# Optimization experiments

Measured on AMD Instinct MI355X. Metric: run time of the kernel, lower is better.

## Reference

```python
import jax, jax.numpy as jnp
import numpy as np

B, T, C, H = 2, 2048, 1024, 16
HD = C // H  # head dim = 64


def setup_inputs() -> dict:
    key = jax.random.key(0)
    k0, k1, k2 = jax.random.split(key, 3)
    x = jax.random.normal(k0, (B, T, C), jnp.float32)
    W_attn = jax.random.normal(k1, (C, 3 * C), jnp.float32) * 0.02
    b_attn = jnp.zeros((3 * C,), jnp.float32)
    W_proj = jax.random.normal(k2, (C, C), jnp.float32) * 0.02
    b_proj = jnp.zeros((C,), jnp.float32)
    # rope: (1,1,T,HD//2,2,2) stack of 2x2 rotation matrices [[cos,-sin],[sin,cos]]
    inv_freq = 1.0 / (10000.0 ** (jnp.arange(0, HD, 2, dtype=jnp.float32) / HD))
    ang = jnp.arange(T, dtype=jnp.float32)[:, None] * inv_freq[None, :]  # (T, HD//2)
    cos, sin = jnp.cos(ang), jnp.sin(ang)
    rope = jnp.stack([jnp.stack([cos, -sin], -1), jnp.stack([sin, cos], -1)], -2)
    rope = rope[None, None]  # (1,1,T,HD//2,2,2)
    return dict(x=x, W_attn=W_attn, b_attn=b_attn, W_proj=W_proj, b_proj=b_proj, rope=rope)


def reference(x, W_attn, b_attn, W_proj, b_proj, rope):
    Bv, Tv, Cv = x.shape
    Hd = Cv // H
    qkv = x @ W_attn + b_attn                      # (B,T,3C) fused QKV proj
    q, k, v = jnp.split(qkv, 3, axis=-1)

    def heads(t):
        return t.reshape(Bv, Tv, H, Hd).transpose(0, 2, 1, 3)  # (B,H,T,Hd)

    q, k, v = heads(q), heads(k), heads(v)

    cos = rope[..., 0, 0][..., None]               # (1,1,T,Hd//2,1)
    sin = rope[..., 1, 0][..., None]

    def rot(t):
        tr = t.reshape(Bv, H, Tv, Hd // 2, 2)
        xr, yr = tr[..., 0:1], tr[..., 1:2]
        out = jnp.concatenate([xr * cos - yr * sin, xr * sin + yr * cos], axis=-1)
        return out.reshape(Bv, H, Tv, Hd)

    q, k = rot(q), rot(k)

    scale = 1.0 / np.sqrt(Hd).astype(np.float32)
    att = jnp.einsum('bhqd,bhkd->bhqk', q, k) * scale
    mask = jnp.tril(jnp.ones((Tv, Tv), dtype=bool))  # causal
    att = jnp.where(mask[None, None], att, -jnp.inf)
    att = jax.nn.softmax(att, axis=-1)
    y = jnp.einsum('bhqk,bhkd->bhqd', att, v)
    y = y.transpose(0, 2, 1, 3).reshape(Bv, Tv, Cv)
    return y @ W_proj + b_proj
```

## Files before the change

### kernel.cpp

```cpp
#include <hip/hip_runtime.h>
#include <hip/hip_bf16.h>

typedef __attribute__((ext_vector_type(8))) short short8;
typedef __attribute__((ext_vector_type(4))) short short4b;
typedef __attribute__((ext_vector_type(4))) float f32x4;
typedef __attribute__((ext_vector_type(16))) float f32x16;
typedef __attribute__((ext_vector_type(4))) unsigned u32x4;

static constexpr int Bb = 2, Tt = 2048, Cc = 1024, Hh = 16;
static constexpr int BT = Bb * Tt;
static constexpr int N1 = 3 * Cc;
static constexpr float QS = 0.125f * 1.44269504f;

__device__ __forceinline__ unsigned short f2b(float f) {
  union { float f; unsigned u; } v; v.f = f;
  unsigned r = v.u + 0x7fffu + ((v.u >> 16) & 1u);
  return (unsigned short)(r >> 16);
}
__device__ __forceinline__ float b2f(short s) {
  union { unsigned u; float f; } v; v.u = ((unsigned)(unsigned short)s) << 16;
  return v.f;
}

__global__ __launch_bounds__(256) void k_cast(const float* __restrict__ in,
                                              unsigned short* __restrict__ out, int n) {
  int i = (blockIdx.x * 256 + threadIdx.x) * 8;
  if (i >= n) return;
  float4 a = *reinterpret_cast<const float4*>(in + i);
  float4 b = *reinterpret_cast<const float4*>(in + i + 4);
  short8 o;
  o[0] = f2b(a.x); o[1] = f2b(a.y); o[2] = f2b(a.z); o[3] = f2b(a.w);
  o[4] = f2b(b.x); o[5] = f2b(b.y); o[6] = f2b(b.z); o[7] = f2b(b.w);
  *reinterpret_cast<short8*>(out + i) = o;
}

__global__ __launch_bounds__(256) void k_tcast(const float* __restrict__ in,
                                               unsigned short* __restrict__ out,
                                               int R, int Ccol) {
  __shared__ float tile[32][33];
  int cb = blockIdx.x * 32, rb = blockIdx.y * 32;
  int tx = threadIdx.x & 31, ty = threadIdx.x >> 5;
  for (int i = 0; i < 32; i += 8)
    tile[ty + i][tx] = in[(size_t)(rb + ty + i) * Ccol + cb + tx];
  __syncthreads();
  for (int i = 0; i < 32; i += 8)
    out[(size_t)(cb + ty + i) * R + rb + tx] = f2b(tile[tx][ty + i]);
}

template <int NF, int EPI>
__global__ __launch_bounds__(512, 2)
void k_gemm8(const unsigned short* __restrict__ A, const unsigned short* __restrict__ Bt,
             const float* __restrict__ bias, void* __restrict__ Cout,
             const float* __restrict__ rope, unsigned short* __restrict__ Qs,
             unsigned short* __restrict__ Ks, unsigned short* __restrict__ Vt,
             int M, int N, int K) {
  constexpr int BN = NF * 64;
  constexpr int ASZ = 256 * 64;
  constexpr int BSZ = BN * 64;
  constexpr int STRIDE = ASZ + BSZ;
  extern __shared__ unsigned short lds[];
  const int tid = threadIdx.x, lane = tid & 63, w = tid >> 6;
  const int wm = w >> 2, wn = w & 3;
  const int l15 = lane & 15, l4 = lane >> 4;
  int nbx = gridDim.x;
  int lin = blockIdx.y * nbx + blockIdx.x;
  int cpx = (nbx * gridDim.y) >> 3;
  lin = (lin & 7) * cpx + (lin >> 3);
  const int mb = lin / nbx, nb = lin % nbx;
  const size_t arow0 = (size_t)mb * 256;
  const size_t brow0 = (size_t)nb * BN;

  const int srow = lane >> 3;
  const int scol = (((lane & 7) * 16) ^ (srow << 4)) >> 1;
  auto stage = [&](int buf, int k0) {
    unsigned short* Ab = lds + buf * STRIDE;
    unsigned short* Bb = Ab + ASZ;
#pragma unroll
    for (int i = 0; i < 4; i++) {
      int c = w + 8 * i;
      const unsigned short* g = A + (arow0 + c * 8 + srow) * (size_t)K + k0 + scol;
      __builtin_amdgcn_global_load_lds((const __attribute__((address_space(1))) void*)g,
          (__attribute__((address_space(3))) void*)(Ab + c * 512), 16, 0, 0);
    }
#pragma unroll
    for (int i = 0; i < NF; i++) {
      int c = w + 8 * i;
      const unsigned short* g = Bt + (brow0 + c * 8 + srow) * (size_t)K + k0 + scol;
      __builtin_amdgcn_global_load_lds((const __attribute__((address_space(1))) void*)g,
          (__attribute__((address_space(3))) void*)(Bb + c * 512), 16, 0, 0);
    }
  };

  f32x4 acc[8][NF] = {};
  const int NK = K >> 6;

  stage(0, 0);
  asm volatile("s_waitcnt vmcnt(0)" ::: "memory");
  asm volatile("s_barrier" ::: "memory");

  for (int kt = 0; kt < NK; kt++) {
    int buf = kt & 1;
    if (kt + 1 < NK) stage(buf ^ 1, (kt + 1) << 6);
    const unsigned short* Ab = lds + buf * STRIDE;
    const unsigned short* Bb = Ab + ASZ;
    short8 af[8][2];
#pragma unroll
    for (int p = 0; p < NF; p++) {
      if (p == 0) {
#pragma unroll
        for (int m = 0; m < 8; m++) {
          int ra = wm * 128 + m * 16 + l15;
#pragma unroll
          for (int kk = 0; kk < 2; kk++) {
            int cb = (kk * 64 + l4 * 16) ^ ((ra & 7) << 4);
            af[m][kk] = *reinterpret_cast<const short8*>(Ab + ra * 64 + (cb >> 1));
          }
        }
      }
      short8 bfr[2];
      int rb = wn * (NF * 16) + p * 16 + l15;
#pragma unroll
      for (int kk = 0; kk < 2; kk++) {
        int cb = (kk * 64 + l4 * 16) ^ ((rb & 7) << 4);
        bfr[kk] = *reinterpret_cast<const short8*>(Bb + rb * 64 + (cb >> 1));
      }
      asm volatile("s_barrier" ::: "memory");
      asm volatile("s_waitcnt lgkmcnt(0)" ::: "memory");
      __builtin_amdgcn_sched_barrier(0);
      __builtin_amdgcn_s_setprio(1);
#pragma unroll
      for (int m = 0; m < 8; m++) {
        acc[m][p] = __builtin_amdgcn_mfma_f32_16x16x32_bf16(af[m][0], bfr[0], acc[m][p], 0, 0, 0);
        acc[m][p] = __builtin_amdgcn_mfma_f32_16x16x32_bf16(af[m][1], bfr[1], acc[m][p], 0, 0, 0);
      }
      __builtin_amdgcn_s_setprio(0);
      if (p == NF - 1)
        asm volatile("s_waitcnt vmcnt(0)" ::: "memory");
      asm volatile("s_barrier" ::: "memory");
    }
  }

#pragma unroll
  for (int m = 0; m < 8; m++) {
#pragma unroll
    for (int n = 0; n < NF; n++) {
      int ccol0 = nb * BN + wn * (NF * 16) + n * 16;
      float bv = bias[ccol0 + l15];
      int r0 = mb * 256 + wm * 128 + m * 16 + l4 * 4;
      if (EPI == 0) {
#pragma unroll
        for (int j = 0; j < 4; j++)
          ((float*)Cout)[(size_t)(r0 + j) * N + ccol0 + l15] = acc[m][n][j] + bv;
      } else {
        int cls = ccol0 >> 10;
        int h = (ccol0 >> 6) & 15;
        int d = (ccol0 & 63) + l15;
        int bq = r0 >> 11;
        int t0 = r0 & 2047;
        size_t bh = (size_t)bq * 16 + h;
        if (cls == 2) {
          short4b o;
#pragma unroll
          for (int j = 0; j < 4; j++) o[j] = (short)f2b(acc[m][n][j] + bv);
          *reinterpret_cast<short4b*>(Vt + (bh * 64 + d) * Tt + t0) = o;
        } else {
          unsigned short* dst = (cls == 0) ? Qs : Ks;
          int jj = d >> 1;
          int odd = d & 1;
#pragma unroll
          for (int j = 0; j < 4; j++) {
            float v = acc[m][n][j] + bv;
            float part = __shfl_xor(v, 1);
            float2 sc = *reinterpret_cast<const float2*>(
                rope + (size_t)(t0 + j) * 128 + jj * 4 + 2);
            float x = odd ? part : v;
            float y = odd ? v : part;
            float rot = odd ? (x * sc.x + y * sc.y)
                            : (x * sc.y - y * sc.x);
            if (cls == 0) rot *= QS;
            dst[(bh * Tt + (t0 + j)) * 64 + d] = f2b(rot);
          }
        }
      }
    }
  }
}

__device__ __forceinline__ float tmax16(const f32x16& v) {
  float a0 = fmaxf(v[0], v[1]),   a1 = fmaxf(v[2], v[3]);
  float a2 = fmaxf(v[4], v[5]),   a3 = fmaxf(v[6], v[7]);
  float a4 = fmaxf(v[8], v[9]),   a5 = fmaxf(v[10], v[11]);
  float a6 = fmaxf(v[12], v[13]), a7 = fmaxf(v[14], v[15]);
  float b0 = fmaxf(a0, a1), b1 = fmaxf(a2, a3), b2 = fmaxf(a4, a5), b3 = fmaxf(a6, a7);
  return fmaxf(fmaxf(b0, b1), fmaxf(b2, b3));
}

template <bool DIAG>
__device__ __forceinline__ void attn_tile128(
    const unsigned short* Kl, const unsigned short* Vl,
    int w, int l31, int hi, const short8 qf[4],
    float& m_run, float& l_run, f32x16 oacc[2]) {
  const int ktmax = DIAG ? w : 3;
  f32x16 s[4];
#pragma unroll
  for (int kt = 0; kt < 4; kt++) {
    if (kt > ktmax) continue;
    f32x16 acc = {};
    int rk = kt * 32 + l31;
    int sw = (rk & 7) << 4;
    const unsigned short* krow = Kl + rk * 64;
    short8 kf[4];
#pragma unroll
    for (int kk = 0; kk < 4; kk++)
      kf[kk] = *reinterpret_cast<const short8*>(krow + (((kk * 32 + hi * 16) ^ sw) >> 1));
    __builtin_amdgcn_s_setprio(1);
#pragma unroll
    for (int kk = 0; kk < 4; kk++)
      acc = __builtin_amdgcn_mfma_f32_32x32x16_bf16(kf[kk], qf[kk], acc, 0, 0, 0);
    __builtin_amdgcn_s_setprio(0);
    if (DIAG && kt == w) {
#pragma unroll
      for (int r = 0; r < 16; r++) {
        int e = (r & 3) + 8 * (r >> 2) + 4 * hi;
        if (e > l31) acc[r] = -1e30f;
      }
    }
    s[kt] = acc;
  }
  float km[4];
#pragma unroll
  for (int kt = 0; kt < 4; kt++) km[kt] = (kt <= ktmax) ? tmax16(s[kt]) : -1e30f;
  float mx = fmaxf(fmaxf(km[0], km[1]), fmaxf(km[2], km[3]));
  mx = fmaxf(mx, __shfl_xor(mx, 32));

  float fsc = 1.f;
  if (!__all(mx <= m_run + 8.f)) {
    float nm = fmaxf(m_run, mx);
    fsc = __builtin_amdgcn_exp2f(m_run - nm);
    m_run = nm;
#pragma unroll
    for (int dt = 0; dt < 2; dt++)
#pragma unroll
      for (int r = 0; r < 16; r++) oacc[dt][r] *= fsc;
  }

  float kps[4] = {0.f, 0.f, 0.f, 0.f};
#pragma unroll
  for (int kt = 0; kt < 4; kt++) {
    if (kt > ktmax) continue;
    float p[16];
#pragma unroll
    for (int r = 0; r < 16; r++) p[r] = __builtin_amdgcn_exp2f(s[kt][r] - m_run);
    float s0 = (p[0] + p[1]) + (p[2] + p[3]);
    float s1 = (p[4] + p[5]) + (p[6] + p[7]);
    float s2 = (p[8] + p[9]) + (p[10] + p[11]);
    float s3 = (p[12] + p[13]) + (p[14] + p[15]);
    kps[kt] = (s0 + s1) + (s2 + s3);
    unsigned P[8];
#pragma unroll
    for (int i = 0; i < 8; i++)
      asm("v_cvt_pk_bf16_f32 %0, %1, %2" : "=v"(P[i]) : "v"(p[2 * i]), "v"(p[2 * i + 1]));
    unsigned Y0 = (unsigned)__shfl_xor((int)(hi ? P[0] : P[2]), 32);
    unsigned Y1 = (unsigned)__shfl_xor((int)(hi ? P[1] : P[3]), 32);
    unsigned Y2 = (unsigned)__shfl_xor((int)(hi ? P[4] : P[6]), 32);
    unsigned Y3 = (unsigned)__shfl_xor((int)(hi ? P[5] : P[7]), 32);
    u32x4 c0 = hi ? u32x4{Y0, Y1, P[2], P[3]} : u32x4{P[0], P[1], Y0, Y1};
    u32x4 c1 = hi ? u32x4{Y2, Y3, P[6], P[7]} : u32x4{P[4], P[5], Y2, Y3};
    short8 pf0 = __builtin_bit_cast(short8, c0);
    short8 pf1 = __builtin_bit_cast(short8, c1);
#pragma unroll
    for (int dt = 0; dt < 2; dt++) {
      int d = dt * 32 + l31;
      int sv = (d & 15) << 4;
      const unsigned short* vrow = Vl + d * 128;
      short8 vf0 = *reinterpret_cast<const short8*>(vrow + (((kt * 64 + hi * 16) ^ sv) >> 1));
      short8 vf1 = *reinterpret_cast<const short8*>(vrow + (((kt * 64 + 32 + hi * 16) ^ sv) >> 1));
      __builtin_amdgcn_s_setprio(1);
      oacc[dt] = __builtin_amdgcn_mfma_f32_32x32x16_bf16(vf0, pf0, oacc[dt], 0, 0, 0);
      oacc[dt] = __builtin_amdgcn_mfma_f32_32x32x16_bf16(vf1, pf1, oacc[dt], 0, 0, 0);
      __builtin_amdgcn_s_setprio(0);
    }
  }
  float psum = (kps[0] + kps[1]) + (kps[2] + kps[3]);
  psum += __shfl_xor(psum, 32);
  l_run = l_run * fsc + psum;
}

__global__ __launch_bounds__(256)
void k_attn(const unsigned short* __restrict__ Qs, const unsigned short* __restrict__ Ks,
            const unsigned short* __restrict__ Vt, unsigned short* __restrict__ Y) {
  __shared__ unsigned short lds[32768];
  int tid = threadIdx.x, lane = tid & 63, w = tid >> 6;
  int s = blockIdx.x;
  int half = s >> 8;
  int p = s & 255;
  int bh = p >> 3;
  int j = p & 7;
  int qb = half ? j : 15 - j;
  int b = bh >> 4, h = bh & 15;
  int l31 = lane & 31, hi = lane >> 5;
  int qw0 = qb * 128 + w * 32;
  const unsigned short* Qb = Qs + (size_t)bh * Tt * 64;
  const unsigned short* Kb = Ks + (size_t)bh * Tt * 64;
  const unsigned short* Vb = Vt + (size_t)bh * 64 * Tt;

  auto stage = [&](int buf, int kv0) {
    unsigned short* Kbuf = lds + buf * 8192;
    unsigned short* Vbuf = lds + 16384 + buf * 8192;
    int krow = lane >> 3;
    int kcolb = ((lane & 7) * 16) ^ ((krow & 7) << 4);
#pragma unroll
    for (int cc = 0; cc < 4; cc++) {
      int c = w + cc * 4;
      const unsigned short* gk = Kb + (size_t)(kv0 + c * 8 + krow) * 64 + (kcolb >> 1);
      __builtin_amdgcn_global_load_lds((const __attribute__((address_space(1))) void*)gk,
          (__attribute__((address_space(3))) void*)(Kbuf + c * 512), 16, 0, 0);
      int vr = c * 4 + (lane >> 4);
      int vcolb = ((lane & 15) * 16) ^ ((vr & 15) << 4);
      const unsigned short* gv = Vb + (size_t)vr * Tt + kv0 + (vcolb >> 1);
      __builtin_amdgcn_global_load_lds((const __attribute__((address_space(1))) void*)gv,
          (__attribute__((address_space(3))) void*)(Vbuf + c * 512), 16, 0, 0);
    }
  };

  short8 qf[4];
#pragma unroll
  for (int kk = 0; kk < 4; kk++)
    qf[kk] = *reinterpret_cast<const short8*>(Qb + (size_t)(qw0 + l31) * 64 + kk * 16 + hi * 8);

  float m_run = -1e30f, l_run = 0.f;
  f32x16 oacc[2] = {};
  const int nt = qb + 1;

  stage(0, 0);
  __syncthreads();
  int cur = 0;
  for (int it = 0; it < nt - 1; ++it) {
    stage(cur ^ 1, (it + 1) * 128);
    attn_tile128<false>(lds + cur * 8192, lds + 16384 + cur * 8192,
                        w, l31, hi, qf, m_run, l_run, oacc);
    __syncthreads();
    cur ^= 1;
  }
  attn_tile128<true>(lds + cur * 8192, lds + 16384 + cur * 8192,
                     w, l31, hi, qf, m_run, l_run, oacc);

  float inv = 1.0f / l_run;
  int t = qw0 + l31;
  unsigned short* yrow = Y + ((size_t)b * Tt + t) * Cc + h * 64;
#pragma unroll
  for (int dt = 0; dt < 2; dt++)
#pragma unroll
    for (int q4 = 0; q4 < 4; q4++) {
      short4b oo;
#pragma unroll
      for (int jj = 0; jj < 4; jj++) oo[jj] = (short)f2b(oacc[dt][q4 * 4 + jj] * inv);
      *reinterpret_cast<short4b*>(yrow + dt * 32 + q4 * 8 + hi * 4) = oo;
    }
}

extern "C" void kernel_launch(void* const* d_in, const int* in_sizes, int n_in,
                              void* d_out, int out_size, void* d_ws, size_t ws_size,
                              hipStream_t stream) {
  (void)in_sizes; (void)n_in; (void)out_size; (void)ws_size;
  const float* x      = (const float*)d_in[0];
  const float* W_attn = (const float*)d_in[1];
  const float* b_attn = (const float*)d_in[2];
  const float* W_proj = (const float*)d_in[3];
  const float* b_proj = (const float*)d_in[4];
  const float* rope   = (const float*)d_in[5];
  float* out = (float*)d_out;

  char* ws = (char*)d_ws;
  unsigned short* xb  = (unsigned short*)(ws);
  unsigned short* WaT = (unsigned short*)(ws + (8u << 20));
  unsigned short* WpT = (unsigned short*)(ws + (14u << 20));
  unsigned short* Qs  = (unsigned short*)(ws + (16u << 20));
  unsigned short* Ks  = (unsigned short*)(ws + (24u << 20));
  unsigned short* Vt  = (unsigned short*)(ws + (32u << 20));
  unsigned short* Yb  = (unsigned short*)(ws + (40u << 20));

  constexpr int LDS_QKV  = (256 + 192) * 64 * 2 * 2;
  constexpr int LDS_PROJ = (256 + 128) * 64 * 2 * 2;
  (void)hipFuncSetAttribute(reinterpret_cast<const void*>(&k_gemm8<3, 1>),
                            hipFuncAttributeMaxDynamicSharedMemorySize, LDS_QKV);
  (void)hipFuncSetAttribute(reinterpret_cast<const void*>(&k_gemm8<2, 0>),
                            hipFuncAttributeMaxDynamicSharedMemorySize, LDS_PROJ);

  k_cast<<<2048, 256, 0, stream>>>(x, xb, BT * Cc);
  k_tcast<<<dim3(N1 / 32, Cc / 32), 256, 0, stream>>>(W_attn, WaT, Cc, N1);
  k_tcast<<<dim3(Cc / 32, Cc / 32), 256, 0, stream>>>(W_proj, WpT, Cc, Cc);
  k_gemm8<3, 1><<<dim3(N1 / 192, BT / 256), 512, LDS_QKV, stream>>>(
      xb, WaT, b_attn, nullptr, rope, Qs, Ks, Vt, BT, N1, Cc);
  k_attn<<<Bb * Hh * (Tt / 128), 256, 0, stream>>>(Qs, Ks, Vt, Yb);
  k_gemm8<2, 0><<<dim3(Cc / 128, BT / 256), 512, LDS_PROJ, stream>>>(
      Yb, WpT, b_proj, out, nullptr, nullptr, nullptr, nullptr, BT, Cc, Cc);
}
```

Measured before the change: 121.6 us.

## Split causal attention KV range across two blocks with separate combine kernel

The attention kernel now splits each query block's causal KV range into two halves processed by separate workgroups (1024 blocks instead of 512). Each writes unnormalized bf16 partial outputs plus running max and sum, and a new combine kernel merges them. The KV tile also drops from 128 to 64 keys, which halves LDS use. The aim is better load balance and occupancy across CUs. In exchange it adds an extra launch, a partial-output round trip through global memory, and extra bf16 rounding of the unnormalized partials.

```diff
diff --git a/kernel.cpp b/kernel.cpp
--- a/kernel.cpp
+++ b/kernel.cpp
@@ -195,16 +195,17 @@
   return fmaxf(fmaxf(b0, b1), fmaxf(b2, b3));
 }
 
-template <bool DIAG>
-__device__ __forceinline__ void attn_tile128(
+__device__ __forceinline__ void attn_tile64(
     const unsigned short* Kl, const unsigned short* Vl,
     int w, int l31, int hi, const short8 qf[4],
-    float& m_run, float& l_run, f32x16 oacc[2]) {
-  const int ktmax = DIAG ? w : 3;
-  f32x16 s[4];
-#pragma unroll
-  for (int kt = 0; kt < 4; kt++) {
-    if (kt > ktmax) continue;
+    float& m_run, float& l_run, f32x16 oacc[2], int grelBase) {
+  f32x16 sc[2];
+  bool act[2];
+#pragma unroll
+  for (int kt = 0; kt < 2; kt++) {
+    int grel = grelBase + kt;
+    act[kt] = (grel <= w);
+    if (!act[kt]) continue;
     f32x16 acc = {};
     int rk = kt * 32 + l31;
     int sw = (rk & 7) << 4;
@@ -218,19 +219,18 @@
     for (int kk = 0; kk < 4; kk++)
       acc = __builtin_amdgcn_mfma_f32_32x32x16_bf16(kf[kk], qf[kk], acc, 0, 0, 0);
     __builtin_amdgcn_s_setprio(0);
-    if (DIAG && kt == w) {
+    if (grel == w) {
 #pragma unroll
       for (int r = 0; r < 16; r++) {
         int e = (r & 3) + 8 * (r >> 2) + 4 * hi;
         if (e > l31) acc[r] = -1e30f;
       }
     }
-    s[kt] = acc;
-  }
-  float km[4];
-#pragma unroll
-  for (int kt = 0; kt < 4; kt++) km[kt] = (kt <= ktmax) ? tmax16(s[kt]) : -1e30f;
-  float mx = fmaxf(fmaxf(km[0], km[1]), fmaxf(km[2], km[3]));
+    sc[kt] = acc;
+  }
+  float km0 = act[0] ? tmax16(sc[0]) : -1e30f;
+  float km1 = act[1] ? tmax16(sc[1]) : -1e30f;
+  float mx = fmaxf(km0, km1);
   mx = fmaxf(mx, __shfl_xor(mx, 32));
 
   float fsc = 1.f;
@@ -244,13 +244,13 @@
       for (int r = 0; r < 16; r++) oacc[dt][r] *= fsc;
   }
 
-  float kps[4] = {0.f, 0.f, 0.f, 0.f};
-#pragma unroll
-  for (int kt = 0; kt < 4; kt++) {
-    if (kt > ktmax) continue;
+  float kps[2] = {0.f, 0.f};
+#pragma unroll
+  for (int kt = 0; kt < 2; kt++) {
+    if (!act[kt]) continue;
     float p[16];
 #pragma unroll
-    for (int r = 0; r < 16; r++) p[r] = __builtin_amdgcn_exp2f(s[kt][r] - m_run);
+    for (int r = 0; r < 16; r++) p[r] = __builtin_amdgcn_exp2f(sc[kt][r] - m_run);
     float s0 = (p[0] + p[1]) + (p[2] + p[3]);
     float s1 = (p[4] + p[5]) + (p[6] + p[7]);
     float s2 = (p[8] + p[9]) + (p[10] + p[11]);
@@ -271,8 +271,8 @@
 #pragma unroll
     for (int dt = 0; dt < 2; dt++) {
       int d = dt * 32 + l31;
-      int sv = (d & 15) << 4;
-      const unsigned short* vrow = Vl + d * 128;
+      int sv = (d & 7) << 4;
+      const unsigned short* vrow = Vl + d * 64;
       short8 vf0 = *reinterpret_cast<const short8*>(vrow + (((kt * 64 + hi * 16) ^ sv) >> 1));
       short8 vf1 = *reinterpret_cast<const short8*>(vrow + (((kt * 64 + 32 + hi * 16) ^ sv) >> 1));
       __builtin_amdgcn_s_setprio(1);
@@ -281,45 +281,46 @@
       __builtin_amdgcn_s_setprio(0);
     }
   }
-  float psum = (kps[0] + kps[1]) + (kps[2] + kps[3]);
+  float psum = kps[0] + kps[1];
   psum += __shfl_xor(psum, 32);
   l_run = l_run * fsc + psum;
 }
 
 __global__ __launch_bounds__(256)
-void k_attn(const unsigned short* __restrict__ Qs, const unsigned short* __restrict__ Ks,
-            const unsigned short* __restrict__ Vt, unsigned short* __restrict__ Y) {
-  __shared__ unsigned short lds[32768];
+void k_attn1(const unsigned short* __restrict__ Qs, const unsigned short* __restrict__ Ks,
+             const unsigned short* __restrict__ Vt, unsigned short* __restrict__ Opart,
+             float* __restrict__ ml) {
+  __shared__ unsigned short lds[16384];
   int tid = threadIdx.x, lane = tid & 63, w = tid >> 6;
-  int s = blockIdx.x;
-  int half = s >> 8;
-  int p = s & 255;
-  int bh = p >> 3;
-  int j = p & 7;
-  int qb = half ? j : 15 - j;
-  int b = bh >> 4, h = bh & 15;
+  int sid = blockIdx.x;
+  int qb = 15 - (sid >> 6);
+  int c = (sid >> 5) & 1;
+  int bh = sid & 31;
   int l31 = lane & 31, hi = lane >> 5;
   int qw0 = qb * 128 + w * 32;
   const unsigned short* Qb = Qs + (size_t)bh * Tt * 64;
   const unsigned short* Kb = Ks + (size_t)bh * Tt * 64;
   const unsigned short* Vb = Vt + (size_t)bh * 64 * Tt;
 
+  const int NT = 2 * qb + 2;
+  const int half = NT >> 1;
+  const int t0 = c ? half : 0;
+  const int t1 = c ? NT : half;
+
   auto stage = [&](int buf, int kv0) {
-    unsigned short* Kbuf = lds + buf * 8192;
-    unsigned short* Vbuf = lds + 16384 + buf * 8192;
-    int krow = lane >> 3;
-    int kcolb = ((lane & 7) * 16) ^ ((krow & 7) << 4);
-#pragma unroll
-    for (int cc = 0; cc < 4; cc++) {
-      int c = w + cc * 4;
-      const unsigned short* gk = Kb + (size_t)(kv0 + c * 8 + krow) * 64 + (kcolb >> 1);
+    unsigned short* Kbuf = lds + buf * 4096;
+    unsigned short* Vbuf = lds + 8192 + buf * 4096;
+    int r8 = lane >> 3;
+    int colb = ((lane & 7) * 16) ^ (r8 << 4);
+#pragma unroll
+    for (int cc = 0; cc < 2; cc++) {
+      int ch = w + cc * 4;
+      const unsigned short* gk = Kb + (size_t)(kv0 + ch * 8 + r8) * 64 + (colb >> 1);
       __builtin_amdgcn_global_load_lds((const __attribute__((address_space(1))) void*)gk,
-          (__attribute__((address_space(3))) void*)(Kbuf + c * 512), 16, 0, 0);
-      int vr = c * 4 + (lane >> 4);
-      int vcolb = ((lane & 15) * 16) ^ ((vr & 15) << 4);
-      const unsigned short* gv = Vb + (size_t)vr * Tt + kv0 + (vcolb >> 1);
+          (__attribute__((address_space(3))) void*)(Kbuf + ch * 512), 16, 0, 0);
+      const unsigned short* gv = Vb + (size_t)(ch * 8 + r8) * Tt + kv0 + (colb >> 1);
       __builtin_amdgcn_global_load_lds((const __attribute__((address_space(1))) void*)gv,
-          (__attribute__((address_space(3))) void*)(Vbuf + c * 512), 16, 0, 0);
+          (__attribute__((address_space(3))) void*)(Vbuf + ch * 512), 16, 0, 0);
     }
   };
 
@@ -330,33 +331,58 @@
 
   float m_run = -1e30f, l_run = 0.f;
   f32x16 oacc[2] = {};
-  const int nt = qb + 1;
-
-  stage(0, 0);
+
+  stage(0, t0 * 64);
   __syncthreads();
   int cur = 0;
-  for (int it = 0; it < nt - 1; ++it) {
-    stage(cur ^ 1, (it + 1) * 128);
-    attn_tile128<false>(lds + cur * 8192, lds + 16384 + cur * 8192,
-                        w, l31, hi, qf, m_run, l_run, oacc);
+  for (int T = t0; T < t1; ++T) {
+    if (T + 1 < t1) stage(cur ^ 1, (T + 1) * 64);
+    attn_tile64(lds + cur * 4096, lds + 8192 + cur * 4096,
+                w, l31, hi, qf, m_run, l_run, oacc, 2 * T - 4 * qb);
     __syncthreads();
     cur ^= 1;
   }
-  attn_tile128<true>(lds + cur * 8192, lds + 16384 + cur * 8192,
-                     w, l31, hi, qf, m_run, l_run, oacc);
-
-  float inv = 1.0f / l_run;
-  int t = qw0 + l31;
-  unsigned short* yrow = Y + ((size_t)b * Tt + t) * Cc + h * 64;
+
+  size_t orow = (size_t)sid * 128 + w * 32 + l31;
 #pragma unroll
   for (int dt = 0; dt < 2; dt++)
 #pragma unroll
     for (int q4 = 0; q4 < 4; q4++) {
       short4b oo;
 #pragma unroll
-      for (int jj = 0; jj < 4; jj++) oo[jj] = (short)f2b(oacc[dt][q4 * 4 + jj] * inv);
-      *reinterpret_cast<short4b*>(yrow + dt * 32 + q4 * 8 + hi * 4) = oo;
-    }
+      for (int jj = 0; jj < 4; jj++) oo[jj] = (short)f2b(oacc[dt][q4 * 4 + jj]);
+      *reinterpret_cast<short4b*>(Opart + orow * 64 + dt * 32 + q4 * 8 + hi * 4) = oo;
+    }
+  if (hi == 0) {
+    float2 v; v.x = m_run; v.y = l_run;
+    *reinterpret_cast<float2*>(ml + orow * 2) = v;
+  }
+}
+
+__global__ __launch_bounds__(256)
+void k_attn2(const unsigned short* __restrict__ Opart, const float* __restrict__ ml,
+             unsigned short* __restrict__ Y) {
+  int gid = blockIdx.x * 256 + threadIdx.x;
+  int row = gid >> 3;
+  int dblk = (gid & 7) * 8;
+  int bh = row >> 11, q = row & 2047;
+  int qb = q >> 7, qrow = q & 127;
+  int s0 = (15 - qb) * 64 + bh;
+  int s1 = s0 + 32;
+  float2 ml0 = *reinterpret_cast<const float2*>(ml + ((size_t)s0 * 128 + qrow) * 2);
+  float2 ml1 = *reinterpret_cast<const float2*>(ml + ((size_t)s1 * 128 + qrow) * 2);
+  float m = fmaxf(ml0.x, ml1.x);
+  float w0 = __builtin_amdgcn_exp2f(ml0.x - m);
+  float w1 = __builtin_amdgcn_exp2f(ml1.x - m);
+  float inv = 1.0f / (w0 * ml0.y + w1 * ml1.y);
+  float a0 = w0 * inv, a1 = w1 * inv;
+  short8 o0 = *reinterpret_cast<const short8*>(Opart + ((size_t)s0 * 128 + qrow) * 64 + dblk);
+  short8 o1 = *reinterpret_cast<const short8*>(Opart + ((size_t)s1 * 128 + qrow) * 64 + dblk);
+  short8 o;
+#pragma unroll
+  for (int j = 0; j < 8; j++) o[j] = (short)f2b(b2f(o0[j]) * a0 + b2f(o1[j]) * a1);
+  int b = bh >> 4, h = bh & 15;
+  *reinterpret_cast<short8*>(Y + ((size_t)(b * Tt + q)) * Cc + h * 64 + dblk) = o;
 }
 
 extern "C" void kernel_launch(void* const* d_in, const int* in_sizes, int n_in,
@@ -372,13 +398,15 @@
   float* out = (float*)d_out;
 
   char* ws = (char*)d_ws;
-  unsigned short* xb  = (unsigned short*)(ws);
-  unsigned short* WaT = (unsigned short*)(ws + (8u << 20));
-  unsigned short* WpT = (unsigned short*)(ws + (14u << 20));
-  unsigned short* Qs  = (unsigned short*)(ws + (16u << 20));
-  unsigned short* Ks  = (unsigned short*)(ws + (24u << 20));
-  unsigned short* Vt  = (unsigned short*)(ws + (32u << 20));
-  unsigned short* Yb  = (unsigned short*)(ws + (40u << 20));
+  unsigned short* xb    = (unsigned short*)(ws);
+  unsigned short* WaT   = (unsigned short*)(ws + (8u << 20));
+  unsigned short* WpT   = (unsigned short*)(ws + (14u << 20));
+  unsigned short* Qs    = (unsigned short*)(ws + (16u << 20));
+  unsigned short* Ks    = (unsigned short*)(ws + (24u << 20));
+  unsigned short* Vt    = (unsigned short*)(ws + (32u << 20));
+  unsigned short* Yb    = (unsigned short*)(ws + (40u << 20));
+  unsigned short* Opart = (unsigned short*)(ws + (48u << 20));
+  float*          ml    = (float*)(ws + (64u << 20));
 
   constexpr int LDS_QKV  = (256 + 192) * 64 * 2 * 2;
   constexpr int LDS_PROJ = (256 + 128) * 64 * 2 * 2;
@@ -392,7 +420,8 @@
   k_tcast<<<dim3(Cc / 32, Cc / 32), 256, 0, stream>>>(W_proj, WpT, Cc, Cc);
   k_gemm8<3, 1><<<dim3(N1 / 192, BT / 256), 512, LDS_QKV, stream>>>(
       xb, WaT, b_attn, nullptr, rope, Qs, Ks, Vt, BT, N1, Cc);
-  k_attn<<<Bb * Hh * (Tt / 128), 256, 0, stream>>>(Qs, Ks, Vt, Yb);
+  k_attn1<<<1024, 256, 0, stream>>>(Qs, Ks, Vt, Opart, ml);
+  k_attn2<<<2048, 256, 0, stream>>>(Opart, ml, Yb);
   k_gemm8<2, 0><<<dim3(Cc / 128, BT / 256), 512, LDS_PROJ, stream>>>(
       Yb, WpT, b_proj, out, nullptr, nullptr, nullptr, nullptr, BT, Cc, Cc);
 }
```

New measurement: 118.2 us. 1.03x faster.
